# Optimization experiments

Hardware: AMD Instinct MI355X
Metric: run time of the kernel (lower is better)

## Reference

```python
import jax, jax.numpy as jnp
import numpy as np

HEAD_DIM = 64
N_HEADS = 16
D_S = N_HEADS * HEAD_DIM  # 1024
D_Z = 128


def setup_inputs() -> dict:
    key = jax.random.key(0)
    ks = jax.random.split(key, 12)
    B, S = 1, 1024
    sc = 0.02
    return {
        "s": jax.random.normal(ks[0], (B, S, D_S), jnp.float32),
        "z": jax.random.normal(ks[1], (B, S, S, D_Z), jnp.float32),
        "wq": jax.random.normal(ks[2], (N_HEADS * HEAD_DIM, D_S), jnp.float32) * sc,
        "bq": jax.random.normal(ks[3], (N_HEADS * HEAD_DIM,), jnp.float32) * sc,
        "wk": jax.random.normal(ks[4], (N_HEADS * HEAD_DIM, D_S), jnp.float32) * sc,
        "wv": jax.random.normal(ks[5], (N_HEADS * HEAD_DIM, D_S), jnp.float32) * sc,
        "wg": jax.random.normal(ks[6], (N_HEADS * HEAD_DIM, D_S), jnp.float32) * sc,
        "z_norm_w": jnp.ones((D_Z,), jnp.float32),
        "z_norm_b": jnp.zeros((D_Z,), jnp.float32),
        "wz": jax.random.normal(ks[7], (N_HEADS, D_Z), jnp.float32) * sc,
        "wo": jax.random.normal(ks[8], (D_S, N_HEADS * HEAD_DIM), jnp.float32) * sc,
    }


def _layer_norm(x, w, b, eps=1e-5):
    mu = jnp.mean(x, axis=-1, keepdims=True)
    var = jnp.var(x, axis=-1, keepdims=True)
    return (x - mu) * jax.lax.rsqrt(var + eps) * w + b


def reference(s, z, wq, bq, wk, wv, wg, z_norm_w, z_norm_b, wz, wo):
    B, S, _ = s.shape
    H, hd = N_HEADS, HEAD_DIM
    # fused QKV projection (only q has bias in the original)
    q = (s @ wq.T + bq).reshape(B, S, H, hd)
    k = (s @ wk.T).reshape(B, S, H, hd)
    v = (s @ wv.T).reshape(B, S, H, hd)
    # pair bias: LN(z) -> linear D_Z -> H, permute to [B,H,S,S]
    zn = _layer_norm(z, z_norm_w, z_norm_b)
    bias = jnp.einsum("bijz,hz->bhij", zn, wz)  # [B,H,S,S]
    # attention with pair bias (net math: qk/sqrt(d) + bias)
    scores = jnp.einsum("bihd,bjhd->bhij", q, k) * (hd ** -0.5) + bias
    attn = jax.nn.softmax(scores, axis=-1)
    o = jnp.einsum("bhij,bjhd->bihd", attn, v).reshape(B, S, H * hd)
    # sigmoid gate then output projection
    g = jax.nn.sigmoid(s @ wg.T)
    return (o * g) @ wo.T
```

## Files before the change

kernel.cpp:

```cpp
#include <hip/hip_runtime.h>

typedef __attribute__((ext_vector_type(8))) short bf16x8;
typedef __attribute__((ext_vector_type(4))) float f32x4;

#define MFMA16(a,b,c) __builtin_amdgcn_mfma_f32_16x16x32_bf16(a,b,c,0,0,0)

__device__ __forceinline__ unsigned short f2bf(float f){
  unsigned int u = __float_as_uint(f);
  unsigned int r = (u + 0x7fffu + ((u >> 16) & 1u)) >> 16;
  return (unsigned short)r;
}
__device__ __forceinline__ float bf2f(unsigned short u){
  return __uint_as_float(((unsigned int)u) << 16);
}
__device__ __forceinline__ bf16x8 cvt8(float4 a, float4 b){
  bf16x8 t;
  t[0] = (short)f2bf(a.x); t[1] = (short)f2bf(a.y);
  t[2] = (short)f2bf(a.z); t[3] = (short)f2bf(a.w);
  t[4] = (short)f2bf(b.x); t[5] = (short)f2bf(b.y);
  t[6] = (short)f2bf(b.z); t[7] = (short)f2bf(b.w);
  return t;
}

__global__ __launch_bounds__(256) void prep_kernel(
    const float* __restrict__ s, const float* __restrict__ wq,
    const float* __restrict__ wk, const float* __restrict__ wv,
    const float* __restrict__ wg, const float* __restrict__ wo,
    const float* __restrict__ wz, const float* __restrict__ znw,
    const float* __restrict__ znb,
    unsigned short* __restrict__ sb, unsigned short* __restrict__ Wp,
    unsigned short* __restrict__ wob,
    unsigned short* __restrict__ wzp, float* __restrict__ c12)
{
  __shared__ float r1[256], r2[256];
  if (blockIdx.x == 6144) {
    int t = threadIdx.x; int h = t >> 4; int k0 = (t & 15) * 8;
    float p1 = 0.f, p2 = 0.f;
    for (int e = 0; e < 8; e++) {
      float wvv = wz[h*128 + k0 + e];
      float w = znw[k0 + e], b = znb[k0 + e];
      wzp[h*128 + k0 + e] = f2bf(wvv * w);
      p1 += wvv * w; p2 += wvv * b;
    }
    r1[t] = p1; r2[t] = p2;
    __syncthreads();
    if ((t & 15) == 0) {
      float s1 = 0.f, s2 = 0.f;
      for (int i = 0; i < 16; i++) { s1 += r1[t + i]; s2 += r2[t + i]; }
      c12[2*h] = s1; c12[2*h + 1] = s2;
    }
    return;
  }
  const size_t M1 = 1u << 20;
  size_t base = ((size_t)blockIdx.x * 256 + threadIdx.x) * 4;
  const float* src; unsigned short* dst; size_t off;
  if (base < M1) { src = s; dst = sb; off = base; }
  else if (base < 5*M1) {
    size_t r = base - M1; int wsel = (int)(r >> 20);
    const float* wsrc0 = (wsel == 0) ? wq : (wsel == 1) ? wk : (wsel == 2) ? wv : wg;
    src = wsrc0; dst = Wp + ((size_t)wsel << 20); off = r & (M1 - 1);
  } else { src = wo; dst = wob; off = base - 5*M1; }
  float4 v = *(const float4*)(src + off);
  ushort4 o4;
  o4.x = f2bf(v.x); o4.y = f2bf(v.y); o4.z = f2bf(v.z); o4.w = f2bf(v.w);
  *(ushort4*)(dst + off) = o4;
}

__global__ __launch_bounds__(256) void bias_gemm(
    const float* __restrict__ z, const unsigned short* __restrict__ wzp,
    const float* __restrict__ c12, unsigned short* __restrict__ bias,
    const unsigned short* __restrict__ sb, const unsigned short* __restrict__ Wp,
    const float* __restrict__ bq,
    unsigned short* __restrict__ qb, unsigned short* __restrict__ kb,
    unsigned short* __restrict__ vT, unsigned short* __restrict__ gb)
{
  __shared__ __align__(16) unsigned short bounce[4][16][20];
  int tid = threadIdx.x;
  int w = tid >> 6, lane = tid & 63;
  int jl = lane & 15, g = lane >> 4;

  if (blockIdx.x < 512) {
    bf16x8 af[4];
    #pragma unroll
    for (int mk = 0; mk < 4; mk++)
      af[mk] = *(const bf16x8*)(wzp + jl*128 + mk*32 + g*8);
    float c1r[4], c2r[4];
    #pragma unroll
    for (int r = 0; r < 4; r++) {
      c1r[r] = c12[2*(g*4 + r)];
      c2r[r] = c12[2*(g*4 + r) + 1];
    }

    int W = blockIdx.x * 4 + w;
    int u0 = W * 32;

    float4 A0[8], A1[8];

    auto loadu = [&](int u, float4 (&A)[8]) {
      int i = u >> 6, j16 = u & 63;
      const float* p = z + ((size_t)i*1024 + j16*16 + jl)*128 + g*8;
      #pragma unroll
      for (int mk = 0; mk < 4; mk++) {
        A[2*mk]   = *(const float4*)(p + mk*32);
        A[2*mk+1] = *(const float4*)(p + mk*32 + 4);
      }
    };
    auto proc = [&](int u, float4 (&A)[8]) {
      float sum = 0.f, sq = 0.f;
      #pragma unroll
      for (int t = 0; t < 8; t++) {
        float4 v = A[t];
        sum += v.x + v.y + v.z + v.w;
        sq = fmaf(v.x, v.x, fmaf(v.y, v.y, fmaf(v.z, v.z, fmaf(v.w, v.w, sq))));
      }
      sum += __shfl_xor(sum, 16); sum += __shfl_xor(sum, 32);
      sq  += __shfl_xor(sq, 16);  sq  += __shfl_xor(sq, 32);
      float mu = sum * (1.f/128.f);
      float rs = rsqrtf(sq * (1.f/128.f) - mu*mu + 1e-5f);
      f32x4 D = {0.f, 0.f, 0.f, 0.f};
      #pragma unroll
      for (int mk = 0; mk < 4; mk++)
        D = MFMA16(af[mk], cvt8(A[2*mk], A[2*mk+1]), D);
      #pragma unroll
      for (int r = 0; r < 4; r++)
        bounce[w][g*4 + r][jl] = f2bf(rs*(D[r] - mu*c1r[r]) + c2r[r]);
      asm volatile("s_waitcnt lgkmcnt(0)" ::: "memory");
      __builtin_amdgcn_sched_barrier(0);
      {
        int i = u >> 6, j16 = u & 63;
        ushort4 vv = *(const ushort4*)(&bounce[w][jl][g*4]);
        *(ushort4*)(bias + ((size_t)jl << 20) + (size_t)i*1024 + j16*16 + g*4) = vv;
      }
      asm volatile("s_waitcnt lgkmcnt(0)" ::: "memory");
      __builtin_amdgcn_sched_barrier(0);
    };

    loadu(u0, A0);
    #pragma unroll 1
    for (int st = 0; st < 32; st += 2) {
      if (st + 1 < 32) loadu(u0 + st + 1, A1);
      proc(u0 + st, A0);
      if (st + 2 < 32) loadu(u0 + st + 2, A0);
      proc(u0 + st + 1, A1);
    }
  } else {
    int bxx = blockIdx.x - 512;
    int bx = bxx & 31, by = bxx >> 5;
    int lr = jl, lg = g;
    int row0 = by * 64 + (w & 1) * 32;
    int col0 = bx * 128 + (w >> 1) * 64;
    f32x4 acc[2][4] = {};
    for (int kk = 0; kk < 1024; kk += 32) {
      bf16x8 afr[2], bfr[4];
      #pragma unroll
      for (int t = 0; t < 2; t++)
        afr[t] = *(const bf16x8*)(sb + (size_t)(row0 + t*16 + lr)*1024 + kk + lg*8);
      #pragma unroll
      for (int t = 0; t < 4; t++)
        bfr[t] = *(const bf16x8*)(Wp + (size_t)(col0 + t*16 + lr)*1024 + kk + lg*8);
      #pragma unroll
      for (int a = 0; a < 2; a++)
        #pragma unroll
        for (int b = 0; b < 4; b++)
          acc[a][b] = MFMA16(afr[a], bfr[b], acc[a][b]);
    }
    #pragma unroll
    for (int a = 0; a < 2; a++)
      #pragma unroll
      for (int b = 0; b < 4; b++)
        #pragma unroll
        for (int r = 0; r < 4; r++) {
          int m = row0 + a*16 + lg*4 + r;
          int n = col0 + b*16 + lr;
          float v = acc[a][b][r];
          if (n < 1024)      { v = (v + bq[n]) * 0.125f; qb[(size_t)m*1024 + n] = f2bf(v); }
          else if (n < 2048) { kb[(size_t)m*1024 + (n-1024)] = f2bf(v); }
          else if (n < 3072) { vT[(size_t)(n-2048)*1024 + m] = f2bf(v); }
          else               { float sg = 1.f / (1.f + __expf(-v)); gb[(size_t)m*1024 + (n-3072)] = f2bf(sg); }
        }
  }
}

__global__ __launch_bounds__(256) void attn_kernel(
    const unsigned short* __restrict__ qb, const unsigned short* __restrict__ kb,
    const unsigned short* __restrict__ vT, const unsigned short* __restrict__ bias,
    const unsigned short* __restrict__ gb, unsigned short* __restrict__ og)
{
  __shared__ unsigned short P[4][1024];
  int lane = threadIdx.x & 63;
  int s = threadIdx.x >> 6;
  int jl = lane & 15, g = lane >> 4;
  int q0 = (blockIdx.x * 4 + s) * 16;
  int h = blockIdx.y;
  unsigned short* Pw = P[s];

  bf16x8 aq[2];
  #pragma unroll
  for (int kh = 0; kh < 2; kh++)
    aq[kh] = *(const bf16x8*)(qb + (size_t)(q0 + jl)*1024 + h*64 + kh*32 + g*8);

  f32x4 od[4] = {};
  float m = -1e30f, ss = 0.f;
  const unsigned short* bp = bias + ((size_t)h << 20);

  for (int jt = 0; jt < 1024; jt += 64) {
    f32x4 sc[4] = {};
    #pragma unroll
    for (int jb = 0; jb < 4; jb++)
      #pragma unroll
      for (int kh = 0; kh < 2; kh++) {
        bf16x8 bk = *(const bf16x8*)(kb + (size_t)(jt + jb*16 + jl)*1024 + h*64 + kh*32 + g*8);
        sc[jb] = MFMA16(bk, aq[kh], sc[jb]);
      }
    #pragma unroll
    for (int jb = 0; jb < 4; jb++) {
      ushort4 bl = *(const ushort4*)(bp + (size_t)(q0 + jl)*1024 + jt + jb*16 + g*4);
      sc[jb][0] += bf2f(bl.x); sc[jb][1] += bf2f(bl.y);
      sc[jb][2] += bf2f(bl.z); sc[jb][3] += bf2f(bl.w);
    }

    float mx = -1e30f;
    #pragma unroll
    for (int jb = 0; jb < 4; jb++)
      #pragma unroll
      for (int r = 0; r < 4; r++) mx = fmaxf(mx, sc[jb][r]);
    mx = fmaxf(mx, __shfl_xor(mx, 16));
    mx = fmaxf(mx, __shfl_xor(mx, 32));
    float mn = fmaxf(m, mx);
    float a = __expf(m - mn);
    m = mn;
    float rsum = 0.f;
    #pragma unroll
    for (int jb = 0; jb < 4; jb++) {
      short4 pk;
      float p0 = __expf(sc[jb][0] - mn); rsum += p0; pk.x = (short)f2bf(p0);
      float p1 = __expf(sc[jb][1] - mn); rsum += p1; pk.y = (short)f2bf(p1);
      float p2 = __expf(sc[jb][2] - mn); rsum += p2; pk.z = (short)f2bf(p2);
      float p3 = __expf(sc[jb][3] - mn); rsum += p3; pk.w = (short)f2bf(p3);
      int b = jb*2 + (g >> 1);
      int bpz = b ^ (jl & 7);
      *(short4*)(Pw + jl*64 + bpz*8 + (g & 1)*4) = pk;
    }
    ss = ss * a + rsum;

    float albc[4];
    #pragma unroll
    for (int r = 0; r < 4; r++) albc[r] = __shfl(a, g*4 + r);
    #pragma unroll
    for (int db = 0; db < 4; db++)
      #pragma unroll
      for (int r = 0; r < 4; r++) od[db][r] *= albc[r];

    #pragma unroll
    for (int jh = 0; jh < 2; jh++) {
      int b = jh*4 + g;
      int bpz = b ^ (jl & 7);
      bf16x8 ap = *(const bf16x8*)(Pw + jl*64 + bpz*8);
      #pragma unroll
      for (int db = 0; db < 4; db++) {
        bf16x8 bv = *(const bf16x8*)(vT + (size_t)(h*64 + db*16 + jl)*1024 + jt + jh*32 + g*8);
        od[db] = MFMA16(ap, bv, od[db]);
      }
    }
  }

  ss += __shfl_xor(ss, 16);
  ss += __shfl_xor(ss, 32);
  float invb[4];
  #pragma unroll
  for (int r = 0; r < 4; r++)
    invb[r] = 1.f / __shfl(ss, g*4 + r);

  #pragma unroll
  for (int db = 0; db < 4; db++)
    #pragma unroll
    for (int r = 0; r < 4; r++) {
      int q = q0 + g*4 + r;
      int d = h*64 + db*16 + jl;
      float gv = bf2f(gb[(size_t)q*1024 + d]);
      og[(size_t)q*1024 + d] = f2bf(od[db][r] * invb[r] * gv);
    }
}

__global__ __launch_bounds__(256) void gemm_out(
    const unsigned short* __restrict__ A, const unsigned short* __restrict__ Bm,
    float* __restrict__ outF)
{
  int lane = threadIdx.x & 63;
  int w = threadIdx.x >> 6;
  int lr = lane & 15, lg = lane >> 4;
  int row0 = blockIdx.y * 64 + (w & 1) * 32;
  int col0 = blockIdx.x * 128 + (w >> 1) * 64;
  f32x4 acc[2][4] = {};
  for (int kk = 0; kk < 1024; kk += 32) {
    bf16x8 af[2], bfr[4];
    #pragma unroll
    for (int t = 0; t < 2; t++)
      af[t] = *(const bf16x8*)(A + (size_t)(row0 + t*16 + lr)*1024 + kk + lg*8);
    #pragma unroll
    for (int t = 0; t < 4; t++)
      bfr[t] = *(const bf16x8*)(Bm + (size_t)(col0 + t*16 + lr)*1024 + kk + lg*8);
    #pragma unroll
    for (int a = 0; a < 2; a++)
      #pragma unroll
      for (int b = 0; b < 4; b++)
        acc[a][b] = MFMA16(af[a], bfr[b], acc[a][b]);
  }
  #pragma unroll
  for (int a = 0; a < 2; a++)
    #pragma unroll
    for (int b = 0; b < 4; b++)
      #pragma unroll
      for (int r = 0; r < 4; r++) {
        int m = row0 + a*16 + lg*4 + r;
        int n = col0 + b*16 + lr;
        outF[(size_t)m * 1024 + n] = acc[a][b][r];
      }
}

extern "C" void kernel_launch(void* const* d_in, const int* in_sizes, int n_in,
                              void* d_out, int out_size, void* d_ws, size_t ws_size,
                              hipStream_t stream) {
  const float* s   = (const float*)d_in[0];
  const float* z   = (const float*)d_in[1];
  const float* wq  = (const float*)d_in[2];
  const float* bq  = (const float*)d_in[3];
  const float* wk  = (const float*)d_in[4];
  const float* wv  = (const float*)d_in[5];
  const float* wg  = (const float*)d_in[6];
  const float* znw = (const float*)d_in[7];
  const float* znb = (const float*)d_in[8];
  const float* wz  = (const float*)d_in[9];
  const float* wo  = (const float*)d_in[10];
  float* out = (float*)d_out;

  char* ws = (char*)d_ws;
  unsigned short* biasb = (unsigned short*)ws;
  unsigned short* qbuf  = (unsigned short*)(ws + ((size_t)64 << 20));
  unsigned short* kbuf  = (unsigned short*)(ws + ((size_t)66 << 20));
  unsigned short* vTb   = (unsigned short*)(ws + ((size_t)68 << 20));
  unsigned short* gbuf  = (unsigned short*)(ws + ((size_t)70 << 20));
  unsigned short* ogb   = (unsigned short*)(ws + ((size_t)72 << 20));
  unsigned short* sb    = (unsigned short*)(ws + ((size_t)74 << 20));
  unsigned short* Wp    = (unsigned short*)(ws + ((size_t)76 << 20));
  unsigned short* wob   = (unsigned short*)(ws + ((size_t)84 << 20));
  unsigned short* wzp   = (unsigned short*)(ws + ((size_t)86 << 20));
  float*          c12   = (float*)(ws + ((size_t)86 << 20) + 4096);

  prep_kernel<<<6145, 256, 0, stream>>>(s, wq, wk, wv, wg, wo, wz, znw, znb,
                                        sb, Wp, wob, wzp, c12);
  bias_gemm<<<1024, 256, 0, stream>>>(z, wzp, c12, biasb,
                                      sb, Wp, bq, qbuf, kbuf, vTb, gbuf);
  attn_kernel<<<dim3(16, 16), 256, 0, stream>>>(qbuf, kbuf, vTb, biasb, gbuf, ogb);
  gemm_out<<<dim3(8, 16), 256, 0, stream>>>(ogb, wob, out);
}
```

Baseline: 255.3 us.

## Split attention over key blocks with combine kernel; reorder bias/QKV blocks

The attention kernel now splits keys across the four warps of each block (split-K), so the grid grows to 64x16 blocks and writes partial outputs plus per-row max and sum to fp32 buffers. A new combine kernel merges the partials with log-sum-exp weights and applies the gate. The fused bias/QKV kernel puts the QKV GEMM blocks first, shrinks per-warp bias work to 16 units with triple buffering and direct scattered stores instead of an LDS bounce, and bf16 conversion uses the library intrinsic. In exchange it adds an extra launch and fp32 partial traffic of about 16 MB, and the bias stores are now narrower.

Result: slower. 265.4 us (+4.0%).

```diff
diff --git a/kernel.cpp b/kernel.cpp
--- a/kernel.cpp
+++ b/kernel.cpp
@@ -1,4 +1,5 @@
 #include <hip/hip_runtime.h>
+#include <hip/hip_bf16.h>
 
 typedef __attribute__((ext_vector_type(8))) short bf16x8;
 typedef __attribute__((ext_vector_type(4))) float f32x4;
@@ -6,9 +7,10 @@
 #define MFMA16(a,b,c) __builtin_amdgcn_mfma_f32_16x16x32_bf16(a,b,c,0,0,0)
 
 __device__ __forceinline__ unsigned short f2bf(float f){
-  unsigned int u = __float_as_uint(f);
-  unsigned int r = (u + 0x7fffu + ((u >> 16) & 1u)) >> 16;
-  return (unsigned short)r;
+  __hip_bfloat16 h = __float2bfloat16(f);
+  unsigned short r;
+  __builtin_memcpy(&r, &h, 2);
+  return r;
 }
 __device__ __forceinline__ float bf2f(unsigned short u){
   return __uint_as_float(((unsigned int)u) << 16);
@@ -66,7 +68,7 @@
   *(ushort4*)(dst + off) = o4;
 }
 
-__global__ __launch_bounds__(256) void bias_gemm(
+__global__ __launch_bounds__(256) void mega1(
     const float* __restrict__ z, const unsigned short* __restrict__ wzp,
     const float* __restrict__ c12, unsigned short* __restrict__ bias,
     const unsigned short* __restrict__ sb, const unsigned short* __restrict__ Wp,
@@ -74,78 +76,12 @@
     unsigned short* __restrict__ qb, unsigned short* __restrict__ kb,
     unsigned short* __restrict__ vT, unsigned short* __restrict__ gb)
 {
-  __shared__ __align__(16) unsigned short bounce[4][16][20];
-  int tid = threadIdx.x;
-  int w = tid >> 6, lane = tid & 63;
+  int lane = threadIdx.x & 63;
+  int w = threadIdx.x >> 6;
   int jl = lane & 15, g = lane >> 4;
 
   if (blockIdx.x < 512) {
-    bf16x8 af[4];
-    #pragma unroll
-    for (int mk = 0; mk < 4; mk++)
-      af[mk] = *(const bf16x8*)(wzp + jl*128 + mk*32 + g*8);
-    float c1r[4], c2r[4];
-    #pragma unroll
-    for (int r = 0; r < 4; r++) {
-      c1r[r] = c12[2*(g*4 + r)];
-      c2r[r] = c12[2*(g*4 + r) + 1];
-    }
-
-    int W = blockIdx.x * 4 + w;
-    int u0 = W * 32;
-
-    float4 A0[8], A1[8];
-
-    auto loadu = [&](int u, float4 (&A)[8]) {
-      int i = u >> 6, j16 = u & 63;
-      const float* p = z + ((size_t)i*1024 + j16*16 + jl)*128 + g*8;
-      #pragma unroll
-      for (int mk = 0; mk < 4; mk++) {
-        A[2*mk]   = *(const float4*)(p + mk*32);
-        A[2*mk+1] = *(const float4*)(p + mk*32 + 4);
-      }
-    };
-    auto proc = [&](int u, float4 (&A)[8]) {
-      float sum = 0.f, sq = 0.f;
-      #pragma unroll
-      for (int t = 0; t < 8; t++) {
-        float4 v = A[t];
-        sum += v.x + v.y + v.z + v.w;
-        sq = fmaf(v.x, v.x, fmaf(v.y, v.y, fmaf(v.z, v.z, fmaf(v.w, v.w, sq))));
-      }
-      sum += __shfl_xor(sum, 16); sum += __shfl_xor(sum, 32);
-      sq  += __shfl_xor(sq, 16);  sq  += __shfl_xor(sq, 32);
-      float mu = sum * (1.f/128.f);
-      float rs = rsqrtf(sq * (1.f/128.f) - mu*mu + 1e-5f);
-      f32x4 D = {0.f, 0.f, 0.f, 0.f};
-      #pragma unroll
-      for (int mk = 0; mk < 4; mk++)
-        D = MFMA16(af[mk], cvt8(A[2*mk], A[2*mk+1]), D);
-      #pragma unroll
-      for (int r = 0; r < 4; r++)
-        bounce[w][g*4 + r][jl] = f2bf(rs*(D[r] - mu*c1r[r]) + c2r[r]);
-      asm volatile("s_waitcnt lgkmcnt(0)" ::: "memory");
-      __builtin_amdgcn_sched_barrier(0);
-      {
-        int i = u >> 6, j16 = u & 63;
-        ushort4 vv = *(const ushort4*)(&bounce[w][jl][g*4]);
-        *(ushort4*)(bias + ((size_t)jl << 20) + (size_t)i*1024 + j16*16 + g*4) = vv;
-      }
-      asm volatile("s_waitcnt lgkmcnt(0)" ::: "memory");
-      __builtin_amdgcn_sched_barrier(0);
-    };
-
-    loadu(u0, A0);
-    #pragma unroll 1
-    for (int st = 0; st < 32; st += 2) {
-      if (st + 1 < 32) loadu(u0 + st + 1, A1);
-      proc(u0 + st, A0);
-      if (st + 2 < 32) loadu(u0 + st + 2, A0);
-      proc(u0 + st + 1, A1);
-    }
-  } else {
-    int bxx = blockIdx.x - 512;
-    int bx = bxx & 31, by = bxx >> 5;
+    int bx = blockIdx.x & 31, by = blockIdx.x >> 5;
     int lr = jl, lg = g;
     int row0 = by * 64 + (w & 1) * 32;
     int col0 = bx * 128 + (w >> 1) * 64;
@@ -178,19 +114,82 @@
           else if (n < 3072) { vT[(size_t)(n-2048)*1024 + m] = f2bf(v); }
           else               { float sg = 1.f / (1.f + __expf(-v)); gb[(size_t)m*1024 + (n-3072)] = f2bf(sg); }
         }
-  }
+    return;
+  }
+
+  bf16x8 af[4];
+  #pragma unroll
+  for (int mk = 0; mk < 4; mk++)
+    af[mk] = *(const bf16x8*)(wzp + jl*128 + mk*32 + g*8);
+  float c1r[4], c2r[4];
+  #pragma unroll
+  for (int r = 0; r < 4; r++) {
+    c1r[r] = c12[2*(g*4 + r)];
+    c2r[r] = c12[2*(g*4 + r) + 1];
+  }
+
+  int W = (blockIdx.x - 512) * 4 + w;
+  int u0 = W * 16;
+
+  float4 RA[8], RB[8], RC[8];
+
+  auto loadu = [&](int k, float4 (&R)[8]) {
+    int u = u0 + k;
+    const float* zp = z + ((size_t)(u >> 6)*1024 + (u & 63)*16 + jl)*128 + g*8;
+    #pragma unroll
+    for (int mk = 0; mk < 4; mk++) {
+      R[2*mk]   = *(const float4*)(zp + mk*32);
+      R[2*mk+1] = *(const float4*)(zp + mk*32 + 4);
+    }
+  };
+  auto procu = [&](int k, float4 (&A)[8]) {
+    int u = u0 + k;
+    float sum = 0.f, sq = 0.f;
+    #pragma unroll
+    for (int q = 0; q < 8; q++) {
+      float4 v = A[q];
+      sum += v.x + v.y + v.z + v.w;
+      sq = fmaf(v.x, v.x, fmaf(v.y, v.y, fmaf(v.z, v.z, fmaf(v.w, v.w, sq))));
+    }
+    sum += __shfl_xor(sum, 16); sum += __shfl_xor(sum, 32);
+    sq  += __shfl_xor(sq, 16);  sq  += __shfl_xor(sq, 32);
+    float mu = sum * (1.f/128.f);
+    float rs = rsqrtf(sq * (1.f/128.f) - mu*mu + 1e-5f);
+    f32x4 D = {0.f, 0.f, 0.f, 0.f};
+    #pragma unroll
+    for (int mk = 0; mk < 4; mk++)
+      D = MFMA16(af[mk], cvt8(A[2*mk], A[2*mk+1]), D);
+    size_t jaddr = (size_t)(u >> 6)*1024 + (u & 63)*16 + jl;
+    #pragma unroll
+    for (int r = 0; r < 4; r++)
+      bias[((size_t)(g*4 + r) << 20) + jaddr] =
+          f2bf(rs*(D[r] - mu*c1r[r]) + c2r[r]);
+  };
+
+  loadu(0, RA);
+  loadu(1, RB);
+  #pragma unroll 1
+  for (int k = 0; k < 15; k += 3) {
+    if (k + 2 < 16) loadu(k + 2, RC);
+    procu(k, RA);
+    if (k + 3 < 16) loadu(k + 3, RA);
+    procu(k + 1, RB);
+    if (k + 4 < 16) loadu(k + 4, RB);
+    if (k + 2 < 16) procu(k + 2, RC);
+  }
+  procu(15, RA);
 }
 
 __global__ __launch_bounds__(256) void attn_kernel(
     const unsigned short* __restrict__ qb, const unsigned short* __restrict__ kb,
     const unsigned short* __restrict__ vT, const unsigned short* __restrict__ bias,
-    const unsigned short* __restrict__ gb, unsigned short* __restrict__ og)
+    float* __restrict__ op, float* __restrict__ ml, float* __restrict__ ll)
 {
   __shared__ unsigned short P[4][1024];
   int lane = threadIdx.x & 63;
   int s = threadIdx.x >> 6;
   int jl = lane & 15, g = lane >> 4;
-  int q0 = (blockIdx.x * 4 + s) * 16;
+  int q0 = blockIdx.x * 16;
   int h = blockIdx.y;
   unsigned short* Pw = P[s];
 
@@ -203,7 +202,7 @@
   float m = -1e30f, ss = 0.f;
   const unsigned short* bp = bias + ((size_t)h << 20);
 
-  for (int jt = 0; jt < 1024; jt += 64) {
+  for (int jt = s*256; jt < s*256 + 256; jt += 64) {
     f32x4 sc[4] = {};
     #pragma unroll
     for (int jb = 0; jb < 4; jb++)
@@ -266,20 +265,62 @@
 
   ss += __shfl_xor(ss, 16);
   ss += __shfl_xor(ss, 32);
-  float invb[4];
-  #pragma unroll
-  for (int r = 0; r < 4; r++)
-    invb[r] = 1.f / __shfl(ss, g*4 + r);
-
+
+  size_t base = ((size_t)(s*16 + h) * 1024);
   #pragma unroll
   for (int db = 0; db < 4; db++)
     #pragma unroll
     for (int r = 0; r < 4; r++) {
       int q = q0 + g*4 + r;
-      int d = h*64 + db*16 + jl;
-      float gv = bf2f(gb[(size_t)q*1024 + d]);
-      og[(size_t)q*1024 + d] = f2bf(od[db][r] * invb[r] * gv);
-    }
+      op[(base + q)*64 + db*16 + jl] = od[db][r];
+    }
+  if (g == 0) {
+    ml[base + q0 + jl] = m;
+    ll[base + q0 + jl] = ss;
+  }
+}
+
+__global__ __launch_bounds__(256) void combine_kernel(
+    const float* __restrict__ op, const float* __restrict__ ml,
+    const float* __restrict__ ll, const unsigned short* __restrict__ gb,
+    unsigned short* __restrict__ og)
+{
+  int t = blockIdx.x * 256 + threadIdx.x;
+  int d4 = t & 15;
+  int q = (t >> 4) & 1023;
+  int h = t >> 14;
+
+  float mv[4], lv[4];
+  float mstar = -1e30f;
+  #pragma unroll
+  for (int s = 0; s < 4; s++) {
+    mv[s] = ml[(size_t)(s*16 + h)*1024 + q];
+    lv[s] = ll[(size_t)(s*16 + h)*1024 + q];
+    mstar = fmaxf(mstar, mv[s]);
+  }
+  float lsum = 0.f;
+  float ws[4];
+  #pragma unroll
+  for (int s = 0; s < 4; s++) {
+    ws[s] = __expf(mv[s] - mstar);
+    lsum = fmaf(ws[s], lv[s], lsum);
+  }
+  float inv = 1.f / lsum;
+
+  float4 o = {0.f, 0.f, 0.f, 0.f};
+  #pragma unroll
+  for (int s = 0; s < 4; s++) {
+    float4 p = *(const float4*)(op + ((size_t)(s*16 + h)*1024 + q)*64 + d4*4);
+    o.x = fmaf(ws[s], p.x, o.x); o.y = fmaf(ws[s], p.y, o.y);
+    o.z = fmaf(ws[s], p.z, o.z); o.w = fmaf(ws[s], p.w, o.w);
+  }
+  ushort4 gv = *(const ushort4*)(gb + (size_t)q*1024 + h*64 + d4*4);
+  ushort4 r;
+  r.x = f2bf(o.x * inv * bf2f(gv.x));
+  r.y = f2bf(o.y * inv * bf2f(gv.y));
+  r.z = f2bf(o.z * inv * bf2f(gv.z));
+  r.w = f2bf(o.w * inv * bf2f(gv.w));
+  *(ushort4*)(og + (size_t)q*1024 + h*64 + d4*4) = r;
 }
 
 __global__ __launch_bounds__(256) void gemm_out(
@@ -346,11 +387,15 @@
   unsigned short* wob   = (unsigned short*)(ws + ((size_t)84 << 20));
   unsigned short* wzp   = (unsigned short*)(ws + ((size_t)86 << 20));
   float*          c12   = (float*)(ws + ((size_t)86 << 20) + 4096);
+  float*          opart = (float*)(ws + ((size_t)96 << 20));
+  float*          mlb   = (float*)(ws + ((size_t)112 << 20));
+  float*          llb   = (float*)(ws + ((size_t)113 << 20));
 
   prep_kernel<<<6145, 256, 0, stream>>>(s, wq, wk, wv, wg, wo, wz, znw, znb,
                                         sb, Wp, wob, wzp, c12);
-  bias_gemm<<<1024, 256, 0, stream>>>(z, wzp, c12, biasb,
-                                      sb, Wp, bq, qbuf, kbuf, vTb, gbuf);
-  attn_kernel<<<dim3(16, 16), 256, 0, stream>>>(qbuf, kbuf, vTb, biasb, gbuf, ogb);
+  mega1<<<1536, 256, 0, stream>>>(z, wzp, c12, biasb,
+                                  sb, Wp, bq, qbuf, kbuf, vTb, gbuf);
+  attn_kernel<<<dim3(64, 16), 256, 0, stream>>>(qbuf, kbuf, vTb, biasb, opart, mlb, llb);
+  combine_kernel<<<1024, 256, 0, stream>>>(opart, mlb, llb, gbuf, ogb);
   gemm_out<<<dim3(8, 16), 256, 0, stream>>>(ogb, wob, out);
 }
```
